# Kernel optimization log

Hardware: AMD Instinct MI355X
Metric: run time of the kernel (lower is better)

Reference implementation:

```python
import jax, jax.numpy as jnp
import numpy as np

H = 12          # heads in the ViT blocks
D = 768         # model dim (hard-coded in the module)
DFF = 3072      # mlp hidden = 4*D
ADIM = 64       # adapter bottleneck dim
L = 32          # num_latents
EPS = 1e-6      # timm ViT LayerNorm eps


def _ln(x, g, b):
    m = jnp.mean(x, axis=-1, keepdims=True)
    v = jnp.var(x, axis=-1, keepdims=True)
    return (x - m) * jax.lax.rsqrt(v + EPS) * g + b


def _quick_gelu(x):
    return x * jax.nn.sigmoid(1.702 * x)


def _sh_attn(q, k, v):
    # single-head attention used by fusion(); scale = C**-0.5 with C = full dim
    C = q.shape[-1]
    a = jax.nn.softmax(jnp.einsum('bnc,bmc->bnm', q, k) * (C ** -0.5), axis=-1)
    return jnp.einsum('bnm,bmc->bnc', a, v)


def _mhsa(x, qkv_w, qkv_b, proj_w, proj_b):
    B, N, C = x.shape
    Dh = C // H
    qkv = (x @ qkv_w.T + qkv_b).reshape(B, N, 3, H, Dh).transpose(2, 0, 3, 1, 4)
    q, k, v = qkv[0], qkv[1], qkv[2]                       # [B,H,N,Dh]
    a = jax.nn.softmax(jnp.einsum('bhnd,bhmd->bhnm', q, k) * (Dh ** -0.5), axis=-1)
    o = jnp.einsum('bhnm,bhmd->bhnd', a, v).transpose(0, 2, 1, 3).reshape(B, N, C)
    return o @ proj_w.T + proj_b


def _stream(t, ln1_g, ln1_b, qkv_w, qkv_b, proj_w, proj_b,
            ln2_g, ln2_b, fc1_w, fc1_b, fc2_w, fc2_b,
            down_w, down_b, up_w, up_b, scale):
    t = t + _mhsa(_ln(t, ln1_g, ln1_b), qkv_w, qkv_b, proj_w, proj_b)
    h = _ln(t, ln2_g, ln2_b)
    mlp = jax.nn.gelu(h @ fc1_w.T + fc1_b, approximate=False) @ fc2_w.T + fc2_b
    adapter = (_quick_gelu(h @ down_w.T + down_b) @ up_w.T + up_b) * scale
    return t + mlp + adapter


def setup_inputs() -> dict:
    key = jax.random.key(0)
    ks = iter(jax.random.split(key, 64))
    f32 = jnp.float32
    def rn(shape, std=0.02):
        return (jax.random.normal(next(ks), shape, dtype=f32) * std)
    inp = {
        'x': jax.random.normal(next(ks), (16, 512, 768), dtype=f32),
        'y': jax.random.normal(next(ks), (16, 196, 768), dtype=f32),
        'latents': rn((1, L, D)),
        'scale_a': jnp.full((1,), 0.5, f32),
        'scale_v': jnp.full((1,), 0.5, f32),
    }
    for p in ('spec', 'rgb'):
        inp.update({
            f'{p}_ln1_g': jnp.ones((D,), f32), f'{p}_ln1_b': jnp.zeros((D,), f32),
            f'{p}_qkv_w': rn((3 * D, D)), f'{p}_qkv_b': jnp.zeros((3 * D,), f32),
            f'{p}_proj_w': rn((D, D)), f'{p}_proj_b': jnp.zeros((D,), f32),
            f'{p}_ln2_g': jnp.ones((D,), f32), f'{p}_ln2_b': jnp.zeros((D,), f32),
            f'{p}_fc1_w': rn((DFF, D)), f'{p}_fc1_b': jnp.zeros((DFF,), f32),
            f'{p}_fc2_w': rn((D, DFF)), f'{p}_fc2_b': jnp.zeros((D,), f32),
            f'{p}_down_w': rn((ADIM, D)), f'{p}_down_b': jnp.zeros((ADIM,), f32),
            f'{p}_up_w': rn((D, ADIM)), f'{p}_up_b': jnp.zeros((D,), f32),
            f'{p}_scale': jnp.ones((1,), f32),
        })
    return inp


def reference(x, y, latents, scale_a, scale_v,
              spec_ln1_g, spec_ln1_b, spec_qkv_w, spec_qkv_b, spec_proj_w, spec_proj_b,
              spec_ln2_g, spec_ln2_b, spec_fc1_w, spec_fc1_b, spec_fc2_w, spec_fc2_b,
              spec_down_w, spec_down_b, spec_up_w, spec_up_b, spec_scale,
              rgb_ln1_g, rgb_ln1_b, rgb_qkv_w, rgb_qkv_b, rgb_proj_w, rgb_proj_b,
              rgb_ln2_g, rgb_ln2_b, rgb_fc1_w, rgb_fc1_b, rgb_fc2_w, rgb_fc2_b,
              rgb_down_w, rgb_down_b, rgb_up_w, rgb_up_b, rgb_scale):
    B = x.shape[0]
    # --- fusion via latent bottleneck (single-head attention) ---
    concat_ = jnp.concatenate((x, y), axis=1)                 # [B, Na+Nv, D]
    lat = jnp.broadcast_to(latents, (B, L, D))
    fused = _sh_attn(lat, concat_, concat_)                   # [B, L, D]
    x = x + scale_a * _sh_attn(x, fused, fused)
    y = y + scale_v * _sh_attn(y, fused, fused)
    # --- per-stream transformer block + adapter (dropout = eval/identity) ---
    x = _stream(x, spec_ln1_g, spec_ln1_b, spec_qkv_w, spec_qkv_b, spec_proj_w, spec_proj_b,
                spec_ln2_g, spec_ln2_b, spec_fc1_w, spec_fc1_b, spec_fc2_w, spec_fc2_b,
                spec_down_w, spec_down_b, spec_up_w, spec_up_b, spec_scale)
    y = _stream(y, rgb_ln1_g, rgb_ln1_b, rgb_qkv_w, rgb_qkv_b, rgb_proj_w, rgb_proj_b,
                rgb_ln2_g, rgb_ln2_b, rgb_fc1_w, rgb_fc1_b, rgb_fc2_w, rgb_fc2_b,
                rgb_down_w, rgb_down_b, rgb_up_w, rgb_up_b, rgb_scale)
    return (x, y)
```

## Files before the change

### kernel.cpp

```cpp
#include <hip/hip_runtime.h>
#include <hip/hip_bf16.h>


#define H_HEADS 12
#define DMODEL 768
#define DFF 3072
#define ADIM 64
#define NLAT 32
#define BATCH 16
#define NA 512
#define NV 196
#define NTOT 708
#define MCAT (BATCH * NTOT)

typedef __hip_bfloat16 bf16;
using bf16x8 = __attribute__((ext_vector_type(8))) short;
using f32x4  = __attribute__((ext_vector_type(4))) float;

static __device__ __forceinline__ float bf2f(bf16 v) { return __bfloat162float(v); }
static __device__ __forceinline__ float bflo(unsigned u) { return __uint_as_float(u << 16); }
static __device__ __forceinline__ float ld1(const float* p) { return *p; }
static __device__ __forceinline__ float ld1(const bf16* p) { return bf2f(*p); }
static __device__ __forceinline__ unsigned short f2bf_bits(float v) {
    unsigned u = __float_as_uint(v);
    return (unsigned short)((u + 0x7fffu + ((u >> 16) & 1u)) >> 16);
}

#define GLD_LDS16(gp, lp) __builtin_amdgcn_global_load_lds( \
    (const __attribute__((address_space(1))) void*)(gp), \
    (__attribute__((address_space(3))) void*)(lp), 16, 0, 0)

static inline int pad8(int v) { return (v + 7) & ~7; }

__global__ void detect_dtype_kernel(const unsigned short* __restrict__ x, int* __restrict__ flag)
{
    if (threadIdx.x == 0 && blockIdx.x == 0) {
        int big = 0;
        for (int i = 0; i < 2048; i++) {
            unsigned e = (x[i] >> 7) & 0xFF;
            if (e >= 0x90) big++;
        }
        flag[0] = (big > 16) ? 1 : 0;
        flag[1] = 0;
    }
}

template<typename TIn>
static __device__ __forceinline__ void pack_body(
    const TIn* __restrict__ x, const TIn* __restrict__ y, const TIn* __restrict__ lat,
    bf16* __restrict__ Cc, bf16* __restrict__ Lb)
{
    const int r = blockIdx.x, tid = threadIdx.x;
    const TIn* src;
    bf16* dst;
    if (r < MCAT) {
        const int b = r / NTOT, n = r - b * NTOT;
        src = (n < NA) ? x + ((size_t)(b * NA + n)) * DMODEL
                       : y + ((size_t)(b * NV + (n - NA))) * DMODEL;
        dst = Cc + (size_t)r * DMODEL;
    } else {
        src = lat + (size_t)(r - MCAT) * DMODEL;
        dst = Lb + (size_t)(r - MCAT) * DMODEL;
    }
    dst[tid]       = __float2bfloat16(ld1(src + tid));
    dst[tid + 256] = __float2bfloat16(ld1(src + tid + 256));
    dst[tid + 512] = __float2bfloat16(ld1(src + tid + 512));
}

__global__ __launch_bounds__(256)
void pack_concat_kernel(const int* __restrict__ flag, const void* x, const void* y,
                        const void* lat, bf16* __restrict__ Cc, bf16* __restrict__ Lb)
{
    if (flag[0]) pack_body<float>((const float*)x, (const float*)y, (const float*)lat, Cc, Lb);
    else         pack_body<bf16>((const bf16*)x, (const bf16*)y, (const bf16*)lat, Cc, Lb);
}

__global__ __launch_bounds__(64)
void fusion_softmax_kernel(const float* __restrict__ scores, float* __restrict__ P)
{
    const int b = blockIdx.x >> 5, l = blockIdx.x & 31, lane = threadIdx.x;
    const float* sp = scores + (size_t)b * NTOT * NLAT + l;
    float v[12];
    float mx = -1e30f;
    #pragma unroll
    for (int i = 0; i < 12; i++) {
        const int n = lane + i * 64;
        v[i] = (n < NTOT) ? sp[(size_t)n * NLAT] * 0.03608439182435161f : -1e30f;
        mx = fmaxf(mx, v[i]);
    }
    #pragma unroll
    for (int off = 32; off; off >>= 1) mx = fmaxf(mx, __shfl_xor(mx, off));
    float den = 0.f;
    #pragma unroll
    for (int i = 0; i < 12; i++) { v[i] = __expf(v[i] - mx); den += v[i]; }
    #pragma unroll
    for (int off = 32; off; off >>= 1) den += __shfl_xor(den, off);
    const float inv = 1.0f / den;
    float* op = P + ((size_t)b * NLAT + l) * 768;
    #pragma unroll
    for (int i = 0; i < 12; i++) {
        const int n = lane + i * 64;
        op[n] = (n < NTOT) ? v[i] * inv : 0.f;
    }
}

__global__ __launch_bounds__(256)
void fusion_wsum_kernel(const bf16* __restrict__ Cc, const float* __restrict__ P,
                        bf16* __restrict__ fused)
{
    const int b = blockIdx.y, d0 = blockIdx.x * 128;
    const int tid = threadIdx.x;
    const int lg = tid >> 5, dg = tid & 31;
    const int l0 = lg * 4;

    __shared__ float Ct[64][132];
    __shared__ float Ps[32][68];

    float acc[4][4] = {};

    for (int nc = 0; nc < 12; nc++) {
        const int n0 = nc * 64;
        __syncthreads();
        #pragma unroll
        for (int it = 0; it < 8; it++) {
            const int idx = it * 1024 + tid * 4;
            const int r = idx >> 7, c = idx & 127;
            const int gn = n0 + r;
            float4 v = make_float4(0.f, 0.f, 0.f, 0.f);
            if (gn < NTOT) {
                const ushort4 u = *(const ushort4*)(Cc + ((size_t)(b * NTOT + gn)) * DMODEL + d0 + c);
                v = make_float4(bflo(u.x), bflo(u.y), bflo(u.z), bflo(u.w));
            }
            Ct[r][c] = v.x; Ct[r][c + 1] = v.y; Ct[r][c + 2] = v.z; Ct[r][c + 3] = v.w;
        }
        {
            const int l = tid >> 3, off = (tid & 7) * 8;
            const float* pp = P + ((size_t)b * NLAT + l) * 768 + n0 + off;
            const float4 p0 = *(const float4*)pp;
            const float4 p1 = *(const float4*)(pp + 4);
            Ps[l][off] = p0.x; Ps[l][off + 1] = p0.y; Ps[l][off + 2] = p0.z; Ps[l][off + 3] = p0.w;
            Ps[l][off + 4] = p1.x; Ps[l][off + 5] = p1.y; Ps[l][off + 6] = p1.z; Ps[l][off + 7] = p1.w;
        }
        __syncthreads();

        for (int n = 0; n < 64; n++) {
            const float4 v = *(const float4*)&Ct[n][dg * 4];
            #pragma unroll
            for (int i = 0; i < 4; i++) {
                const float p = Ps[l0 + i][n];
                acc[i][0] += p * v.x; acc[i][1] += p * v.y;
                acc[i][2] += p * v.z; acc[i][3] += p * v.w;
            }
        }
    }

    #pragma unroll
    for (int i = 0; i < 4; i++) {
        bf16* op = fused + ((size_t)b * NLAT + l0 + i) * DMODEL + d0 + dg * 4;
        #pragma unroll
        for (int j = 0; j < 4; j++) op[j] = __float2bfloat16(acc[i][j]);
    }
}

template<typename TIn>
static __device__ __forceinline__ void attend_fused_body(
    const TIn* __restrict__ t, const bf16* __restrict__ fused,
    const TIn* __restrict__ scale_p, const TIn* __restrict__ lng, const TIn* __restrict__ lnb,
    bf16* __restrict__ out, bf16* __restrict__ hout, int Npb)
{
    const int tid = threadIdx.x;
    const int gid = blockIdx.x;
    const int b = gid / Npb;
    const TIn* row = t + (size_t)gid * DMODEL;
    const bf16* fb = fused + (size_t)b * NLAT * DMODEL;

    __shared__ float q[DMODEL];
    __shared__ float p[NLAT];
    __shared__ float rs[4], rq[4];

    for (int d = tid; d < DMODEL; d += 256) q[d] = ld1(row + d);
    __syncthreads();

    const int g = tid >> 3, li = tid & 7;
    float s = 0.f;
    const bf16* fr = fb + (size_t)g * DMODEL;
    for (int d = li; d < DMODEL; d += 8) s += q[d] * bf2f(fr[d]);
    s += __shfl_xor(s, 1); s += __shfl_xor(s, 2); s += __shfl_xor(s, 4);
    if (li == 0) p[g] = s * 0.03608439182435161f;
    __syncthreads();

    float mx = -1e30f;
    #pragma unroll
    for (int l = 0; l < NLAT; l++) mx = fmaxf(mx, p[l]);
    float w[NLAT];
    float den = 0.f;
    #pragma unroll
    for (int l = 0; l < NLAT; l++) { w[l] = __expf(p[l] - mx); den += w[l]; }
    const float sA = ld1(scale_p) / den;

    float a0 = 0.f, a1 = 0.f, a2 = 0.f;
    #pragma unroll
    for (int l = 0; l < NLAT; l++) {
        const bf16* fv = fb + (size_t)l * DMODEL;
        a0 += w[l] * bf2f(fv[tid]);
        a1 += w[l] * bf2f(fv[tid + 256]);
        a2 += w[l] * bf2f(fv[tid + 512]);
    }
    const float t0v = q[tid] + sA * a0;
    const float t1v = q[tid + 256] + sA * a1;
    const float t2v = q[tid + 512] + sA * a2;
    bf16* o = out + (size_t)gid * DMODEL;
    o[tid]       = __float2bfloat16(t0v);
    o[tid + 256] = __float2bfloat16(t1v);
    o[tid + 512] = __float2bfloat16(t2v);

    if (hout) {
        float ss = t0v + t1v + t2v;
        float sq = t0v * t0v + t1v * t1v + t2v * t2v;
        #pragma unroll
        for (int off = 32; off; off >>= 1) { ss += __shfl_xor(ss, off); sq += __shfl_xor(sq, off); }
        if ((tid & 63) == 0) { rs[tid >> 6] = ss; rq[tid >> 6] = sq; }
        __syncthreads();
        ss = rs[0] + rs[1] + rs[2] + rs[3];
        sq = rq[0] + rq[1] + rq[2] + rq[3];
        const float mean = ss * (1.0f / DMODEL);
        const float var = sq * (1.0f / DMODEL) - mean * mean;
        const float r = rsqrtf(var + 1e-6f);
        bf16* ho = hout + (size_t)gid * DMODEL;
        ho[tid]       = __float2bfloat16((t0v - mean) * r * ld1(lng + tid)       + ld1(lnb + tid));
        ho[tid + 256] = __float2bfloat16((t1v - mean) * r * ld1(lng + tid + 256) + ld1(lnb + tid + 256));
        ho[tid + 512] = __float2bfloat16((t2v - mean) * r * ld1(lng + tid + 512) + ld1(lnb + tid + 512));
    }
}

__global__ __launch_bounds__(256)
void attend_fused_kernel(const int* __restrict__ flag, const void* t, const bf16* __restrict__ fused,
                         const void* scale_p, const void* lng, const void* lnb,
                         bf16* __restrict__ out, bf16* __restrict__ hout, int Npb)
{
    if (flag[0]) attend_fused_body<float>((const float*)t, fused, (const float*)scale_p,
                                          (const float*)lng, (const float*)lnb, out, hout, Npb);
    else         attend_fused_body<bf16>((const bf16*)t, fused, (const bf16*)scale_p,
                                         (const bf16*)lng, (const bf16*)lnb, out, hout, Npb);
}

template<typename TW>
static __device__ __forceinline__ void ln_body(
    const bf16* __restrict__ in, const TW* __restrict__ g,
    const TW* __restrict__ bta, bf16* __restrict__ out)
{
    const int tid = threadIdx.x;
    const bf16* p = in + (size_t)blockIdx.x * DMODEL;
    const float v0 = bf2f(p[tid]), v1 = bf2f(p[tid + 256]), v2 = bf2f(p[tid + 512]);
    float s = v0 + v1 + v2;
    float sq = v0 * v0 + v1 * v1 + v2 * v2;
    #pragma unroll
    for (int off = 32; off; off >>= 1) { s += __shfl_xor(s, off); sq += __shfl_xor(sq, off); }
    __shared__ float rs[4], rq[4];
    if ((tid & 63) == 0) { rs[tid >> 6] = s; rq[tid >> 6] = sq; }
    __syncthreads();
    s = rs[0] + rs[1] + rs[2] + rs[3];
    sq = rq[0] + rq[1] + rq[2] + rq[3];
    const float mean = s * (1.0f / DMODEL);
    const float var = sq * (1.0f / DMODEL) - mean * mean;
    const float r = rsqrtf(var + 1e-6f);
    bf16* o = out + (size_t)blockIdx.x * DMODEL;
    o[tid]       = __float2bfloat16((v0 - mean) * r * ld1(g + tid)       + ld1(bta + tid));
    o[tid + 256] = __float2bfloat16((v1 - mean) * r * ld1(g + tid + 256) + ld1(bta + tid + 256));
    o[tid + 512] = __float2bfloat16((v2 - mean) * r * ld1(g + tid + 512) + ld1(bta + tid + 512));
}

__global__ __launch_bounds__(256)
void ln_kernel(const int* __restrict__ flag, const bf16* __restrict__ in,
               const void* g, const void* b, bf16* __restrict__ out)
{
    if (flag[0]) ln_body<float>(in, (const float*)g, (const float*)b, out);
    else         ln_body<bf16>(in, (const bf16*)g, (const bf16*)b, out);
}

__global__ __launch_bounds__(256)
void flash_attn_kernel(const bf16* __restrict__ qkv, bf16* __restrict__ o, int Npb)
{
    const int tid = threadIdx.x;
    const int wv = tid >> 6, lane = tid & 63;
    const int l15 = lane & 15, q4 = lane >> 4;
    const int h = blockIdx.x % H_HEADS, bb = blockIdx.x / H_HEADS;
    const int qt = blockIdx.y;
    const int nkv = (Npb + 63) >> 6;
    const size_t tokbase = (size_t)bb * Npb;

    __shared__ __align__(16) short Ks[64 * 64];
    __shared__ __align__(16) short Vt[64 * 64];
    __shared__ __align__(16) short Ps[4][16 * 64];

    const int qr = min(qt * 64 + wv * 16 + l15, Npb - 1);
    const bf16* qp = qkv + (tokbase + qr) * 2304 + h * 64;
    const bf16x8 qf0 = *(const bf16x8*)(const void*)(qp + q4 * 8);
    const bf16x8 qf1 = *(const bf16x8*)(const void*)(qp + 32 + q4 * 8);

    f32x4 Oa[4] = {};
    float mrow[4], lrow[4];
    #pragma unroll
    for (int i = 0; i < 4; i++) { mrow[i] = -1e30f; lrow[i] = 0.f; }

    for (int kv = 0; kv < nkv; kv++) {
        const int kv0 = kv * 64;
        __syncthreads();
        #pragma unroll
        for (int inst = 0; inst < 2; inst++) {
            const int s = inst * 256 + tid;
            const int row = s >> 3, pos = s & 7;
            const int c = pos ^ (row & 7);
            const int krc = min(kv0 + row, Npb - 1);
            GLD_LDS16(qkv + (tokbase + krc) * 2304 + DMODEL + h * 64 + c * 8, &Ks[s * 8]);
        }
        {
            const int r = tid >> 2;
            const int f0 = (tid & 3) * 16;
            const int krc = min(kv0 + r, Npb - 1);
            const short* vp = (const short*)(qkv + (tokbase + krc) * 2304 + 2 * DMODEL + h * 64 + f0);
            short vb[16];
            *(uint4*)&vb[0] = *(const uint4*)vp;
            *(uint4*)&vb[8] = *(const uint4*)(vp + 8);
            const int chunk = r >> 3, r7 = r & 7;
            #pragma unroll
            for (int j = 0; j < 16; j++) {
                const int feat = f0 + j;
                Vt[feat * 64 + (chunk ^ (feat & 7)) * 8 + r7] = vb[j];
            }
        }
        __syncthreads();

        f32x4 s4[4] = {};
        #pragma unroll
        for (int kk = 0; kk < 2; kk++) {
            const bf16x8 qf = kk ? qf1 : qf0;
            const int c = kk * 4 + q4;
            #pragma unroll
            for (int g = 0; g < 4; g++) {
                const int r = g * 16 + l15;
                const bf16x8 kf = *(const bf16x8*)(const void*)&Ks[r * 64 + (c ^ (r & 7)) * 8];
                s4[g] = __builtin_amdgcn_mfma_f32_16x16x32_bf16(qf, kf, s4[g], 0, 0, 0);
            }
        }
        float tmax[4];
        #pragma unroll
        for (int i = 0; i < 4; i++) tmax[i] = -1e30f;
        #pragma unroll
        for (int g = 0; g < 4; g++) {
            const bool valid = (kv0 + g * 16 + l15) < Npb;
            #pragma unroll
            for (int i = 0; i < 4; i++) {
                const float v = s4[g][i] * 0.125f;
                s4[g][i] = valid ? v : -1e30f;
                tmax[i] = fmaxf(tmax[i], s4[g][i]);
            }
        }
        #pragma unroll
        for (int off = 1; off < 16; off <<= 1)
            #pragma unroll
            for (int i = 0; i < 4; i++) tmax[i] = fmaxf(tmax[i], __shfl_xor(tmax[i], off));
        float alpha[4], rsum[4];
        #pragma unroll
        for (int i = 0; i < 4; i++) {
            const float mn = fmaxf(mrow[i], tmax[i]);
            alpha[i] = __expf(mrow[i] - mn);
            mrow[i] = mn;
            rsum[i] = 0.f;
        }
        #pragma unroll
        for (int g = 0; g < 4; g++) {
            const int cc = g * 16 + l15;
            const int chunk = cc >> 3;
            #pragma unroll
            for (int i = 0; i < 4; i++) {
                const int r = q4 * 4 + i;
                const float p = __expf(s4[g][i] - mrow[i]);
                rsum[i] += p;
                Ps[wv][r * 64 + (chunk ^ (r & 7)) * 8 + (cc & 7)] = (short)f2bf_bits(p);
            }
        }
        #pragma unroll
        for (int off = 1; off < 16; off <<= 1)
            #pragma unroll
            for (int i = 0; i < 4; i++) rsum[i] += __shfl_xor(rsum[i], off);
        #pragma unroll
        for (int i = 0; i < 4; i++) lrow[i] = lrow[i] * alpha[i] + rsum[i];
        #pragma unroll
        for (int g = 0; g < 4; g++)
            #pragma unroll
            for (int i = 0; i < 4; i++) Oa[g][i] *= alpha[i];

        #pragma unroll
        for (int kk = 0; kk < 2; kk++) {
            const int c = kk * 4 + q4;
            const bf16x8 pf = *(const bf16x8*)(const void*)&Ps[wv][l15 * 64 + (c ^ (l15 & 7)) * 8];
            #pragma unroll
            for (int g = 0; g < 4; g++) {
                const int feat = g * 16 + l15;
                const bf16x8 vf = *(const bf16x8*)(const void*)&Vt[feat * 64 + (c ^ (feat & 7)) * 8];
                Oa[g] = __builtin_amdgcn_mfma_f32_16x16x32_bf16(pf, vf, Oa[g], 0, 0, 0);
            }
        }
    }

    float inv[4];
    #pragma unroll
    for (int i = 0; i < 4; i++) inv[i] = 1.0f / lrow[i];
    #pragma unroll
    for (int g = 0; g < 4; g++) {
        const int colo = h * 64 + g * 16 + l15;
        #pragma unroll
        for (int i = 0; i < 4; i++) {
            const int rowg = qt * 64 + wv * 16 + q4 * 4 + i;
            if (rowg < Npb)
                o[(tokbase + rowg) * DMODEL + colo] = __float2bfloat16(Oa[g][i] * inv[i]);
        }
    }
}

template<int TM, int ACT, bool RES, bool SCALE, bool FD, typename TW>
static __device__ __forceinline__ void gemm_body(
    const bf16* __restrict__ A, const TW* __restrict__ W, const TW* __restrict__ Wd,
    const TW* __restrict__ bias, const TW* __restrict__ biasd,
    const bf16* __restrict__ resid, const TW* __restrict__ scale_p,
    void* __restrict__ C, bf16* __restrict__ Cd,
    bool cf32, int row_off, int M, int N, int K, short* As, short* Bs)
{
    const int tid = threadIdx.x;
    const int lane = tid & 63;
    const int wv = tid >> 6;
    const int l15 = lane & 15, q4 = lane >> 4;
    const int m0 = blockIdx.x * TM, n0 = blockIdx.y * 128;
    const int N1 = FD ? N - ADIM : N;
    constexpr int NF = (TM == 128) ? 4 : 2;
    const int wm = (TM == 128) ? (wv & 1) * 64 : 0;
    const int wn = (TM == 128) ? (wv >> 1) * 64 : wv * 32;

    f32x4 acc[4][NF] = {};

    for (int k0 = 0; k0 < K; k0 += 64) {
        __syncthreads();
        constexpr int AIT = TM * 8 / 256;
        #pragma unroll
        for (int it = 0; it < AIT; it++) {
            const int i = it * 256 + tid;
            const int row = i >> 3, pos = i & 7;
            const int c = pos ^ (row & 7);
            const int ra = min(m0 + row, M - 1);
            GLD_LDS16(A + (size_t)ra * K + k0 + c * 8, &As[i * 8]);
        }
        #pragma unroll
        for (int it = 0; it < 4; it++) {
            const int i = it * 256 + tid;
            const int row = i >> 3, pos = i & 7;
            const int c = pos ^ (row & 7);
            const int rb = min(n0 + row, N - 1);
            const TW* wp = (FD && rb >= N1) ? Wd + (size_t)(rb - N1) * K
                                            : W + (size_t)rb * K;
            if constexpr (sizeof(TW) == 2) {
                GLD_LDS16(wp + k0 + c * 8, &Bs[i * 8]);
            } else {
                const float* fp = (const float*)wp + k0 + c * 8;
                const float4 w0 = *(const float4*)fp;
                const float4 w1 = *(const float4*)(fp + 4);
                unsigned short hb[8];
                hb[0] = f2bf_bits(w0.x); hb[1] = f2bf_bits(w0.y);
                hb[2] = f2bf_bits(w0.z); hb[3] = f2bf_bits(w0.w);
                hb[4] = f2bf_bits(w1.x); hb[5] = f2bf_bits(w1.y);
                hb[6] = f2bf_bits(w1.z); hb[7] = f2bf_bits(w1.w);
                *(uint4*)&Bs[i * 8] = *(const uint4*)hb;
            }
        }
        __syncthreads();

        #pragma unroll
        for (int kk = 0; kk < 2; kk++) {
            bf16x8 af[4], bfr[NF];
            #pragma unroll
            for (int f = 0; f < 4; f++) {
                const int r = wm + f * 16 + l15;
                af[f] = *(const bf16x8*)(const void*)&As[(r * 8 + ((kk * 4 + q4) ^ (r & 7))) * 8];
            }
            #pragma unroll
            for (int g = 0; g < NF; g++) {
                const int rn = wn + g * 16 + l15;
                bfr[g] = *(const bf16x8*)(const void*)&Bs[(rn * 8 + ((kk * 4 + q4) ^ (rn & 7))) * 8];
            }
            #pragma unroll
            for (int f = 0; f < 4; f++)
                #pragma unroll
                for (int g = 0; g < NF; g++)
                    acc[f][g] = __builtin_amdgcn_mfma_f32_16x16x32_bf16(af[f], bfr[g], acc[f][g], 0, 0, 0);
        }
    }

    const float sc = SCALE ? ld1(scale_p) : 1.0f;
    #pragma unroll
    for (int g = 0; g < NF; g++) {
        const int colg = n0 + wn + g * 16 + l15;
        if (colg >= N) continue;
        const bool isdown = FD && (colg >= N1);
        const float bv = bias ? (isdown ? ld1(biasd + colg - N1) : ld1(bias + colg)) : 0.f;
        #pragma unroll
        for (int f = 0; f < 4; f++) {
            const int rowb = m0 + wm + f * 16 + q4 * 4;
            #pragma unroll
            for (int i = 0; i < 4; i++) {
                const int rowg = rowb + i;
                if (rowg >= M) continue;
                float v = acc[f][g][i] + bv;
                if (FD) {
                    if (isdown) v = v / (1.0f + __expf(-1.702f * v));
                    else v = 0.5f * v * (1.0f + erff(v * 0.70710678118654752f));
                } else if (ACT == 1) v = 0.5f * v * (1.0f + erff(v * 0.70710678118654752f));
                else if (ACT == 2) v = v / (1.0f + __expf(-1.702f * v));
                if (SCALE) v *= sc;
                if (RES) v += bf2f(resid[(size_t)rowg * N + colg]);
                if (FD && isdown) {
                    Cd[(size_t)rowg * ADIM + (colg - N1)] = __float2bfloat16(v);
                } else {
                    const size_t sidx = (size_t)(rowg + row_off) * N1 + colg;
                    if (cf32) ((float*)C)[sidx] = v;
                    else ((bf16*)C)[sidx] = __float2bfloat16(v);
                }
            }
        }
    }
}

template<int TM, int ACT, bool RES, bool SCALE, bool FD>
__global__ __launch_bounds__(256)
void mfma_gemm_kernel(const int* __restrict__ flag, const bf16* __restrict__ A,
                      const void* __restrict__ W, const void* __restrict__ Wd,
                      const void* __restrict__ bias, const void* __restrict__ biasd,
                      const bf16* __restrict__ resid, const void* __restrict__ sp,
                      void* __restrict__ C, bf16* __restrict__ Cd,
                      int out_mode, int row_off, int M, int N, int K)
{
    __shared__ __align__(16) short As[TM * 64];
    __shared__ __align__(16) short Bs[128 * 64];
    if (blockIdx.x * TM >= M) return;
    const bool cf32 = (out_mode == 2) || (out_mode == 1 && flag[0] != 0);
    if (flag[0])
        gemm_body<TM, ACT, RES, SCALE, FD, float>(A, (const float*)W, (const float*)Wd,
            (const float*)bias, (const float*)biasd, resid, (const float*)sp, C, Cd,
            cf32, row_off, M, N, K, As, Bs);
    else
        gemm_body<TM, ACT, RES, SCALE, FD, bf16>(A, (const bf16*)W, (const bf16*)Wd,
            (const bf16*)bias, (const bf16*)biasd, resid, (const bf16*)sp, C, Cd,
            cf32, row_off, M, N, K, As, Bs);
}

struct SW {
    const void *ln1_g, *ln1_b, *qkv_w, *qkv_b, *proj_w, *proj_b,
               *ln2_g, *ln2_b, *fc1_w, *fc1_b, *fc2_w, *fc2_b,
               *down_w, *down_b, *up_w, *up_b, *scale;
};

static void run_stream(const int* flag, bf16* t0, int M, int Npb, int nb, const SW& w,
                       bf16* h, bf16* big, bf16* ah, void* out, int out_row_off,
                       bool skip_ln1, hipStream_t s)
{
    const int mt128 = pad8((M + 127) / 128);
    const int mt64  = pad8((M + 63) / 64);
    const dim3 gqkv(mt128, 18);
    const dim3 gfc1(mt128, 25);
    const dim3 g768(mt64, 6);

    if (!skip_ln1) ln_kernel<<<M, 256, 0, s>>>(flag, t0, w.ln1_g, w.ln1_b, h);
    mfma_gemm_kernel<128, 0, false, false, false><<<gqkv, 256, 0, s>>>(
        flag, h, w.qkv_w, nullptr, w.qkv_b, nullptr, nullptr, nullptr, big, nullptr,
        0, 0, M, 2304, DMODEL);
    flash_attn_kernel<<<dim3(nb * H_HEADS, (Npb + 63) / 64), 256, 0, s>>>(big, h, Npb);
    mfma_gemm_kernel<64, 0, true, false, false><<<g768, 256, 0, s>>>(
        flag, h, w.proj_w, nullptr, w.proj_b, nullptr, t0, nullptr, t0, nullptr,
        0, 0, M, DMODEL, DMODEL);
    ln_kernel<<<M, 256, 0, s>>>(flag, t0, w.ln2_g, w.ln2_b, h);
    mfma_gemm_kernel<128, 1, false, false, true><<<gfc1, 256, 0, s>>>(
        flag, h, w.fc1_w, w.down_w, w.fc1_b, w.down_b, nullptr, nullptr, big, ah,
        0, 0, M, DFF + ADIM, DMODEL);
    mfma_gemm_kernel<64, 0, true, false, false><<<g768, 256, 0, s>>>(
        flag, big, w.fc2_w, nullptr, w.fc2_b, nullptr, t0, nullptr, t0, nullptr,
        0, 0, M, DMODEL, DFF);
    mfma_gemm_kernel<64, 0, true, true, false><<<g768, 256, 0, s>>>(
        flag, ah, w.up_w, nullptr, w.up_b, nullptr, t0, w.scale, out, nullptr,
        1, out_row_off, M, DMODEL, ADIM);
}

extern "C" void kernel_launch(void* const* d_in, const int* in_sizes, int n_in,
                              void* d_out, int out_size, void* d_ws, size_t ws_size,
                              hipStream_t stream)
{
    SW sw, rw;
    auto fill = [&](SW& s, int base) {
        s.ln1_g = d_in[base + 0];  s.ln1_b = d_in[base + 1];
        s.qkv_w = d_in[base + 2];  s.qkv_b = d_in[base + 3];
        s.proj_w = d_in[base + 4]; s.proj_b = d_in[base + 5];
        s.ln2_g = d_in[base + 6];  s.ln2_b = d_in[base + 7];
        s.fc1_w = d_in[base + 8];  s.fc1_b = d_in[base + 9];
        s.fc2_w = d_in[base + 10]; s.fc2_b = d_in[base + 11];
        s.down_w = d_in[base + 12]; s.down_b = d_in[base + 13];
        s.up_w = d_in[base + 14];  s.up_b = d_in[base + 15];
        s.scale = d_in[base + 16];
    };
    fill(sw, 5);
    fill(rw, 22);

    const int Mx = BATCH * NA;
    const int My = BATCH * NV;

    int* flag = (int*)d_ws;
    char* base = (char*)d_ws + 256;
    bf16* x1 = (bf16*)base;                base += (size_t)Mx * DMODEL * 2;
    bf16* y1 = (bf16*)base;                base += (size_t)My * DMODEL * 2;
    bf16* fused = (bf16*)base;             base += (size_t)BATCH * NLAT * DMODEL * 2;
    char* un = base;

    bf16* Cc = (bf16*)un;
    bf16* Lb = (bf16*)(un + (size_t)MCAT * DMODEL * 2);
    float* scores = (float*)(un + (size_t)(MCAT + 64) * DMODEL * 2);
    float* P = (float*)((char*)scores + (size_t)MCAT * NLAT * 4 + 256);

    const size_t stream_need_big = ((size_t)Mx * DMODEL + (size_t)Mx * DFF + (size_t)Mx * ADIM) * 2;
    const size_t fixed = 256 + ((size_t)Mx * DMODEL + (size_t)My * DMODEL + (size_t)BATCH * NLAT * DMODEL) * 2;
    const bool big_ws = ws_size >= fixed + stream_need_big;
    const int hrows = big_ws ? Mx : My;
    bf16* h  = (bf16*)un;
    bf16* big = h + (size_t)hrows * DMODEL;
    bf16* ah = big + (size_t)hrows * DFF;

    detect_dtype_kernel<<<1, 64, 0, stream>>>((const unsigned short*)d_in[0], flag);

    pack_concat_kernel<<<MCAT + NLAT, 256, 0, stream>>>(flag, d_in[0], d_in[1], d_in[2], Cc, Lb);
    mfma_gemm_kernel<128, 0, false, false, false><<<dim3(pad8((MCAT + 127) / 128), 1), 256, 0, stream>>>(
        flag + 1, Cc, Lb, nullptr, nullptr, nullptr, nullptr, nullptr, scores, nullptr,
        2, 0, MCAT, NLAT, DMODEL);
    fusion_softmax_kernel<<<BATCH * NLAT, 64, 0, stream>>>(scores, P);
    fusion_wsum_kernel<<<dim3(DMODEL / 128, BATCH), 256, 0, stream>>>(Cc, P, fused);

    attend_fused_kernel<<<BATCH * NA, 256, 0, stream>>>(
        flag, d_in[0], fused, d_in[3], sw.ln1_g, sw.ln1_b, x1, big_ws ? h : nullptr, NA);
    if (big_ws) {
        run_stream(flag, x1, Mx, NA, BATCH, sw, h, big, ah, d_out, 0, true, stream);
    } else {
        const int MCH = 2048;
        for (int c = 0; c < Mx / MCH; c++)
            run_stream(flag, x1 + (size_t)c * MCH * DMODEL, MCH, NA, MCH / NA, sw,
                       h, big, ah, d_out, c * MCH, false, stream);
    }

    attend_fused_kernel<<<BATCH * NV, 256, 0, stream>>>(
        flag, d_in[1], fused, d_in[4], rw.ln1_g, rw.ln1_b, y1, h, NV);
    run_stream(flag, y1, My, NV, BATCH, rw, h, big, ah, d_out, Mx, true, stream);
}
```

Before: 1.349 ms.

## Batch x and y streams into merged GEMM launches and stage epilogue through LDS

Concatenates the audio and visual token streams into one buffer so each GEMM, LayerNorm and MLP launch covers both. Blocks pick their weights by row index against a split point, which removes half the launches and the tail effects of the smaller y stream. The GEMM epilogue now writes through a swizzled LDS buffer, giving vectorised 4-wide coalesced stores and residual loads. The cost is a larger workspace requirement with fallback paths, plus extra LDS synchronisation in the epilogue.

```diff
diff --git a/kernel.cpp b/kernel.cpp
--- a/kernel.cpp
+++ b/kernel.cpp
@@ -12,6 +12,7 @@
 #define NV 196
 #define NTOT 708
 #define MCAT (BATCH * NTOT)
+#define MTOT (BATCH * (NA + NV))
 
 typedef __hip_bfloat16 bf16;
 using bf16x8 = __attribute__((ext_vector_type(8))) short;
@@ -272,8 +273,12 @@
 
 __global__ __launch_bounds__(256)
 void ln_kernel(const int* __restrict__ flag, const bf16* __restrict__ in,
-               const void* g, const void* b, bf16* __restrict__ out)
-{
+               const void* g0, const void* b0, const void* g1, const void* b1,
+               bf16* __restrict__ out, int split)
+{
+    const bool isY = (int)blockIdx.x >= split;
+    const void* g = isY ? g1 : g0;
+    const void* b = isY ? b1 : b0;
     if (flag[0]) ln_body<float>(in, (const float*)g, (const float*)b, out);
     else         ln_body<bf16>(in, (const bf16*)g, (const bf16*)b, out);
 }
@@ -425,7 +430,8 @@
     const TW* __restrict__ bias, const TW* __restrict__ biasd,
     const bf16* __restrict__ resid, const TW* __restrict__ scale_p,
     void* __restrict__ C, bf16* __restrict__ Cd,
-    bool cf32, int row_off, int M, int N, int K, short* As, short* Bs)
+    bool cf32, int row_off, int M, int N, int K,
+    short* As, short* Bs, float* Ep)
 {
     const int tid = threadIdx.x;
     const int lane = tid & 63;
@@ -456,8 +462,7 @@
             const int row = i >> 3, pos = i & 7;
             const int c = pos ^ (row & 7);
             const int rb = min(n0 + row, N - 1);
-            const TW* wp = (FD && rb >= N1) ? Wd + (size_t)(rb - N1) * K
-                                            : W + (size_t)rb * K;
+            const TW* wp = (FD && rb >= N1) ? Wd + (size_t)(rb - N1) * K : W + (size_t)rb * K;
             if constexpr (sizeof(TW) == 2) {
                 GLD_LDS16(wp + k0 + c * 8, &Bs[i * 8]);
             } else {
@@ -494,62 +499,101 @@
                     acc[f][g] = __builtin_amdgcn_mfma_f32_16x16x32_bf16(af[f], bfr[g], acc[f][g], 0, 0, 0);
         }
     }
+    __syncthreads();
 
     const float sc = SCALE ? ld1(scale_p) : 1.0f;
-    #pragma unroll
-    for (int g = 0; g < NF; g++) {
-        const int colg = n0 + wn + g * 16 + l15;
-        if (colg >= N) continue;
-        const bool isdown = FD && (colg >= N1);
-        const float bv = bias ? (isdown ? ld1(biasd + colg - N1) : ld1(bias + colg)) : 0.f;
-        #pragma unroll
-        for (int f = 0; f < 4; f++) {
-            const int rowb = m0 + wm + f * 16 + q4 * 4;
-            #pragma unroll
-            for (int i = 0; i < 4; i++) {
-                const int rowg = rowb + i;
-                if (rowg >= M) continue;
-                float v = acc[f][g][i] + bv;
-                if (FD) {
-                    if (isdown) v = v / (1.0f + __expf(-1.702f * v));
-                    else v = 0.5f * v * (1.0f + erff(v * 0.70710678118654752f));
-                } else if (ACT == 1) v = 0.5f * v * (1.0f + erff(v * 0.70710678118654752f));
-                else if (ACT == 2) v = v / (1.0f + __expf(-1.702f * v));
-                if (SCALE) v *= sc;
-                if (RES) v += bf2f(resid[(size_t)rowg * N + colg]);
-                if (FD && isdown) {
-                    Cd[(size_t)rowg * ADIM + (colg - N1)] = __float2bfloat16(v);
+    constexpr int NPASS = (TM == 128) ? 2 : 1;
+    #pragma unroll
+    for (int pass = 0; pass < NPASS; pass++) {
+        if (wm == pass * 64) {
+            #pragma unroll
+            for (int g = 0; g < NF; g++) {
+                const int col = wn + g * 16 + l15;
+                const int colg = n0 + col;
+                const bool isdown = FD && (colg >= N1);
+                const float bv = bias ? (isdown ? ld1(biasd + (colg - N1)) : ld1(bias + colg)) : 0.f;
+                #pragma unroll
+                for (int f = 0; f < 4; f++) {
+                    #pragma unroll
+                    for (int i = 0; i < 4; i++) {
+                        const int row = f * 16 + q4 * 4 + i;
+                        float v = acc[f][g][i] + bv;
+                        if (FD) {
+                            if (isdown) v = v / (1.0f + __expf(-1.702f * v));
+                            else v = 0.5f * v * (1.0f + erff(v * 0.70710678118654752f));
+                        } else if (ACT == 1) v = 0.5f * v * (1.0f + erff(v * 0.70710678118654752f));
+                        else if (ACT == 2) v = v / (1.0f + __expf(-1.702f * v));
+                        if (SCALE) v *= sc;
+                        const int c = col >> 2;
+                        Ep[row * 128 + (((c ^ (row & 31))) << 2) + (col & 3)] = v;
+                    }
+                }
+            }
+        }
+        __syncthreads();
+        #pragma unroll
+        for (int it = 0; it < 8; it++) {
+            const int cid = it * 256 + tid;
+            const int row = cid >> 5, c = cid & 31;
+            const int rowg = m0 + pass * 64 + row;
+            const int colg = n0 + c * 4;
+            if (rowg < M && colg < N) {
+                f32x4 v = *(const f32x4*)&Ep[row * 128 + (((c ^ (row & 31))) << 2)];
+                if (FD && colg >= N1) {
+                    ushort4 u;
+                    u.x = f2bf_bits(v[0]); u.y = f2bf_bits(v[1]);
+                    u.z = f2bf_bits(v[2]); u.w = f2bf_bits(v[3]);
+                    *(ushort4*)(Cd + (size_t)rowg * ADIM + (colg - N1)) = u;
                 } else {
-                    const size_t sidx = (size_t)(rowg + row_off) * N1 + colg;
-                    if (cf32) ((float*)C)[sidx] = v;
-                    else ((bf16*)C)[sidx] = __float2bfloat16(v);
+                    if (RES) {
+                        const ushort4 r4 = *(const ushort4*)(resid + (size_t)rowg * N + colg);
+                        v[0] += bflo(r4.x); v[1] += bflo(r4.y);
+                        v[2] += bflo(r4.z); v[3] += bflo(r4.w);
+                    }
+                    if (cf32) {
+                        *(f32x4*)((float*)C + (size_t)(rowg + row_off) * N + colg) = v;
+                    } else {
+                        ushort4 u;
+                        u.x = f2bf_bits(v[0]); u.y = f2bf_bits(v[1]);
+                        u.z = f2bf_bits(v[2]); u.w = f2bf_bits(v[3]);
+                        *(ushort4*)((bf16*)C + (size_t)(rowg + row_off) * (FD ? N1 : N) + colg) = u;
+                    }
                 }
             }
         }
+        if (pass + 1 < NPASS) __syncthreads();
     }
 }
 
 template<int TM, int ACT, bool RES, bool SCALE, bool FD>
 __global__ __launch_bounds__(256)
 void mfma_gemm_kernel(const int* __restrict__ flag, const bf16* __restrict__ A,
-                      const void* __restrict__ W, const void* __restrict__ Wd,
-                      const void* __restrict__ bias, const void* __restrict__ biasd,
-                      const bf16* __restrict__ resid, const void* __restrict__ sp,
+                      const void* W0, const void* W1, const void* Wd0, const void* Wd1,
+                      const void* b0, const void* b1, const void* bd0, const void* bd1,
+                      const bf16* __restrict__ resid, const void* sp0, const void* sp1,
                       void* __restrict__ C, bf16* __restrict__ Cd,
-                      int out_mode, int row_off, int M, int N, int K)
-{
-    __shared__ __align__(16) short As[TM * 64];
-    __shared__ __align__(16) short Bs[128 * 64];
-    if (blockIdx.x * TM >= M) return;
+                      int out_mode, int row_off, int M, int N, int K, int split)
+{
+    __shared__ __align__(16) char SMEM[32768];
+    if ((int)blockIdx.x * TM >= M) return;
+    const bool isY = ((int)blockIdx.x * TM) >= split;
+    const void* W = isY ? W1 : W0;
+    const void* Wd = isY ? Wd1 : Wd0;
+    const void* bb = isY ? b1 : b0;
+    const void* bd = isY ? bd1 : bd0;
+    const void* sp = isY ? sp1 : sp0;
+    short* As = (short*)SMEM;
+    short* Bs = As + TM * 64;
+    float* Ep = (float*)SMEM;
     const bool cf32 = (out_mode == 2) || (out_mode == 1 && flag[0] != 0);
     if (flag[0])
         gemm_body<TM, ACT, RES, SCALE, FD, float>(A, (const float*)W, (const float*)Wd,
-            (const float*)bias, (const float*)biasd, resid, (const float*)sp, C, Cd,
-            cf32, row_off, M, N, K, As, Bs);
+            (const float*)bb, (const float*)bd, resid, (const float*)sp, C, Cd,
+            cf32, row_off, M, N, K, As, Bs, Ep);
     else
         gemm_body<TM, ACT, RES, SCALE, FD, bf16>(A, (const bf16*)W, (const bf16*)Wd,
-            (const bf16*)bias, (const bf16*)biasd, resid, (const bf16*)sp, C, Cd,
-            cf32, row_off, M, N, K, As, Bs);
+            (const bf16*)bb, (const bf16*)bd, resid, (const bf16*)sp, C, Cd,
+            cf32, row_off, M, N, K, As, Bs, Ep);
 }
 
 struct SW {
@@ -558,34 +602,35 @@
                *down_w, *down_b, *up_w, *up_b, *scale;
 };
 
-static void run_stream(const int* flag, bf16* t0, int M, int Npb, int nb, const SW& w,
-                       bf16* h, bf16* big, bf16* ah, void* out, int out_row_off,
-                       bool skip_ln1, hipStream_t s)
-{
-    const int mt128 = pad8((M + 127) / 128);
-    const int mt64  = pad8((M + 63) / 64);
-    const dim3 gqkv(mt128, 18);
-    const dim3 gfc1(mt128, 25);
-    const dim3 g768(mt64, 6);
-
-    if (!skip_ln1) ln_kernel<<<M, 256, 0, s>>>(flag, t0, w.ln1_g, w.ln1_b, h);
-    mfma_gemm_kernel<128, 0, false, false, false><<<gqkv, 256, 0, s>>>(
-        flag, h, w.qkv_w, nullptr, w.qkv_b, nullptr, nullptr, nullptr, big, nullptr,
-        0, 0, M, 2304, DMODEL);
-    flash_attn_kernel<<<dim3(nb * H_HEADS, (Npb + 63) / 64), 256, 0, s>>>(big, h, Npb);
-    mfma_gemm_kernel<64, 0, true, false, false><<<g768, 256, 0, s>>>(
-        flag, h, w.proj_w, nullptr, w.proj_b, nullptr, t0, nullptr, t0, nullptr,
-        0, 0, M, DMODEL, DMODEL);
-    ln_kernel<<<M, 256, 0, s>>>(flag, t0, w.ln2_g, w.ln2_b, h);
-    mfma_gemm_kernel<128, 1, false, false, true><<<gfc1, 256, 0, s>>>(
-        flag, h, w.fc1_w, w.down_w, w.fc1_b, w.down_b, nullptr, nullptr, big, ah,
-        0, 0, M, DFF + ADIM, DMODEL);
-    mfma_gemm_kernel<64, 0, true, false, false><<<g768, 256, 0, s>>>(
-        flag, big, w.fc2_w, nullptr, w.fc2_b, nullptr, t0, nullptr, t0, nullptr,
-        0, 0, M, DMODEL, DFF);
-    mfma_gemm_kernel<64, 0, true, true, false><<<g768, 256, 0, s>>>(
-        flag, ah, w.up_w, nullptr, w.up_b, nullptr, t0, w.scale, out, nullptr,
-        1, out_row_off, M, DMODEL, ADIM);
+static void stream_seq(const int* flag, bf16* t0, bf16* h, bf16* big, bf16* ah,
+                       int M, int split, const SW& a, const SW& b,
+                       void* outC, int row_off,
+                       int npb0, int rows0, int npb1, int rows1, hipStream_t s)
+{
+    const dim3 gq(pad8((M + 127) / 128), 18);
+    const dim3 gf(pad8((M + 127) / 128), 25);
+    const dim3 g7(pad8((M + 63) / 64), 6);
+
+    mfma_gemm_kernel<128, 0, false, false, false><<<gq, 256, 0, s>>>(flag, h,
+        a.qkv_w, b.qkv_w, nullptr, nullptr, a.qkv_b, b.qkv_b, nullptr, nullptr,
+        nullptr, nullptr, nullptr, big, nullptr, 0, 0, M, 2304, DMODEL, split);
+    flash_attn_kernel<<<dim3((rows0 / npb0) * H_HEADS, (npb0 + 63) / 64), 256, 0, s>>>(big, h, npb0);
+    if (rows1)
+        flash_attn_kernel<<<dim3((rows1 / npb1) * H_HEADS, (npb1 + 63) / 64), 256, 0, s>>>(
+            big + (size_t)rows0 * 2304, h + (size_t)rows0 * DMODEL, npb1);
+    mfma_gemm_kernel<64, 0, true, false, false><<<g7, 256, 0, s>>>(flag, h,
+        a.proj_w, b.proj_w, nullptr, nullptr, a.proj_b, b.proj_b, nullptr, nullptr,
+        t0, nullptr, nullptr, t0, nullptr, 0, 0, M, DMODEL, DMODEL, split);
+    ln_kernel<<<M, 256, 0, s>>>(flag, t0, a.ln2_g, a.ln2_b, b.ln2_g, b.ln2_b, h, split);
+    mfma_gemm_kernel<128, 1, false, false, true><<<gf, 256, 0, s>>>(flag, h,
+        a.fc1_w, b.fc1_w, a.down_w, b.down_w, a.fc1_b, b.fc1_b, a.down_b, b.down_b,
+        nullptr, nullptr, nullptr, big, ah, 0, 0, M, DFF + ADIM, DMODEL, split);
+    mfma_gemm_kernel<64, 0, true, false, false><<<g7, 256, 0, s>>>(flag, big,
+        a.fc2_w, b.fc2_w, nullptr, nullptr, a.fc2_b, b.fc2_b, nullptr, nullptr,
+        t0, nullptr, nullptr, t0, nullptr, 0, 0, M, DMODEL, DFF, split);
+    mfma_gemm_kernel<64, 0, true, true, false><<<g7, 256, 0, s>>>(flag, ah,
+        a.up_w, b.up_w, nullptr, nullptr, a.up_b, b.up_b, nullptr, nullptr,
+        t0, a.scale, b.scale, outC, nullptr, 1, row_off, M, DMODEL, ADIM, split);
 }
 
 extern "C" void kernel_launch(void* const* d_in, const int* in_sizes, int n_in,
@@ -609,48 +654,105 @@
 
     const int Mx = BATCH * NA;
     const int My = BATCH * NV;
+    const int NOSPLIT = 1 << 30;
+
+    const size_t szA = 256 + ((size_t)MTOT * DMODEL * 2 + (size_t)BATCH * NLAT * DMODEL
+                     + (size_t)MTOT * DFF + (size_t)MTOT * ADIM) * 2;
+    const size_t szB = 256 + ((size_t)Mx * DMODEL * 2 + (size_t)My * DMODEL
+                     + (size_t)BATCH * NLAT * DMODEL + (size_t)Mx * DFF + (size_t)Mx * ADIM) * 2;
 
     int* flag = (int*)d_ws;
-    char* base = (char*)d_ws + 256;
-    bf16* x1 = (bf16*)base;                base += (size_t)Mx * DMODEL * 2;
-    bf16* y1 = (bf16*)base;                base += (size_t)My * DMODEL * 2;
-    bf16* fused = (bf16*)base;             base += (size_t)BATCH * NLAT * DMODEL * 2;
-    char* un = base;
-
-    bf16* Cc = (bf16*)un;
-    bf16* Lb = (bf16*)(un + (size_t)MCAT * DMODEL * 2);
-    float* scores = (float*)(un + (size_t)(MCAT + 64) * DMODEL * 2);
-    float* P = (float*)((char*)scores + (size_t)MCAT * NLAT * 4 + 256);
-
-    const size_t stream_need_big = ((size_t)Mx * DMODEL + (size_t)Mx * DFF + (size_t)Mx * ADIM) * 2;
-    const size_t fixed = 256 + ((size_t)Mx * DMODEL + (size_t)My * DMODEL + (size_t)BATCH * NLAT * DMODEL) * 2;
-    const bool big_ws = ws_size >= fixed + stream_need_big;
-    const int hrows = big_ws ? Mx : My;
-    bf16* h  = (bf16*)un;
-    bf16* big = h + (size_t)hrows * DMODEL;
-    bf16* ah = big + (size_t)hrows * DFF;
-
     detect_dtype_kernel<<<1, 64, 0, stream>>>((const unsigned short*)d_in[0], flag);
 
-    pack_concat_kernel<<<MCAT + NLAT, 256, 0, stream>>>(flag, d_in[0], d_in[1], d_in[2], Cc, Lb);
-    mfma_gemm_kernel<128, 0, false, false, false><<<dim3(pad8((MCAT + 127) / 128), 1), 256, 0, stream>>>(
-        flag + 1, Cc, Lb, nullptr, nullptr, nullptr, nullptr, nullptr, scores, nullptr,
-        2, 0, MCAT, NLAT, DMODEL);
-    fusion_softmax_kernel<<<BATCH * NLAT, 64, 0, stream>>>(scores, P);
-    fusion_wsum_kernel<<<dim3(DMODEL / 128, BATCH), 256, 0, stream>>>(Cc, P, fused);
-
-    attend_fused_kernel<<<BATCH * NA, 256, 0, stream>>>(
-        flag, d_in[0], fused, d_in[3], sw.ln1_g, sw.ln1_b, x1, big_ws ? h : nullptr, NA);
-    if (big_ws) {
-        run_stream(flag, x1, Mx, NA, BATCH, sw, h, big, ah, d_out, 0, true, stream);
+    if (ws_size >= szA) {
+        char* base = (char*)d_ws + 256;
+        bf16* t0 = (bf16*)base;      base += (size_t)MTOT * DMODEL * 2;
+        bf16* fused = (bf16*)base;   base += (size_t)BATCH * NLAT * DMODEL * 2;
+        bf16* h = (bf16*)base;       base += (size_t)MTOT * DMODEL * 2;
+        bf16* big = (bf16*)base;     base += (size_t)MTOT * DFF * 2;
+        bf16* ah = (bf16*)base;
+
+        bf16* Cc = h;
+        bf16* Lb = ah;
+        float* scores = (float*)big;
+        float* P = (float*)((char*)big + 2 * 1024 * 1024);
+
+        pack_concat_kernel<<<MCAT + NLAT, 256, 0, stream>>>(flag, d_in[0], d_in[1], d_in[2], Cc, Lb);
+        mfma_gemm_kernel<128, 0, false, false, false><<<dim3(pad8((MCAT + 127) / 128), 1), 256, 0, stream>>>(
+            flag + 1, Cc, Lb, Lb, nullptr, nullptr, nullptr, nullptr, nullptr, nullptr,
+            nullptr, nullptr, nullptr, scores, nullptr, 2, 0, MCAT, NLAT, DMODEL, NOSPLIT);
+        fusion_softmax_kernel<<<BATCH * NLAT, 64, 0, stream>>>(scores, P);
+        fusion_wsum_kernel<<<dim3(DMODEL / 128, BATCH), 256, 0, stream>>>(Cc, P, fused);
+
+        attend_fused_kernel<<<BATCH * NA, 256, 0, stream>>>(
+            flag, d_in[0], fused, d_in[3], sw.ln1_g, sw.ln1_b, t0, h, NA);
+        attend_fused_kernel<<<BATCH * NV, 256, 0, stream>>>(
+            flag, d_in[1], fused, d_in[4], rw.ln1_g, rw.ln1_b,
+            t0 + (size_t)Mx * DMODEL, h + (size_t)Mx * DMODEL, NV);
+
+        stream_seq(flag, t0, h, big, ah, MTOT, Mx, sw, rw, d_out, 0,
+                   NA, Mx, NV, My, stream);
+    } else if (ws_size >= szB) {
+        char* base = (char*)d_ws + 256;
+        bf16* x1 = (bf16*)base;      base += (size_t)Mx * DMODEL * 2;
+        bf16* y1 = (bf16*)base;      base += (size_t)My * DMODEL * 2;
+        bf16* fused = (bf16*)base;   base += (size_t)BATCH * NLAT * DMODEL * 2;
+        bf16* h = (bf16*)base;       base += (size_t)Mx * DMODEL * 2;
+        bf16* big = (bf16*)base;     base += (size_t)Mx * DFF * 2;
+        bf16* ah = (bf16*)base;
+
+        bf16* Cc = big;
+        bf16* Lb = ah;
+        float* scores = (float*)((char*)big + 18 * 1024 * 1024);
+        float* P = (float*)((char*)big + 20 * 1024 * 1024);
+
+        pack_concat_kernel<<<MCAT + NLAT, 256, 0, stream>>>(flag, d_in[0], d_in[1], d_in[2], Cc, Lb);
+        mfma_gemm_kernel<128, 0, false, false, false><<<dim3(pad8((MCAT + 127) / 128), 1), 256, 0, stream>>>(
+            flag + 1, Cc, Lb, Lb, nullptr, nullptr, nullptr, nullptr, nullptr, nullptr,
+            nullptr, nullptr, nullptr, scores, nullptr, 2, 0, MCAT, NLAT, DMODEL, NOSPLIT);
+        fusion_softmax_kernel<<<BATCH * NLAT, 64, 0, stream>>>(scores, P);
+        fusion_wsum_kernel<<<dim3(DMODEL / 128, BATCH), 256, 0, stream>>>(Cc, P, fused);
+
+        attend_fused_kernel<<<BATCH * NA, 256, 0, stream>>>(
+            flag, d_in[0], fused, d_in[3], sw.ln1_g, sw.ln1_b, x1, h, NA);
+        stream_seq(flag, x1, h, big, ah, Mx, NOSPLIT, sw, sw, d_out, 0, NA, Mx, 0, 0, stream);
+
+        attend_fused_kernel<<<BATCH * NV, 256, 0, stream>>>(
+            flag, d_in[1], fused, d_in[4], rw.ln1_g, rw.ln1_b, y1, h, NV);
+        stream_seq(flag, y1, h, big, ah, My, NOSPLIT, rw, rw, d_out, Mx, NV, My, 0, 0, stream);
     } else {
+        char* base = (char*)d_ws + 256;
+        bf16* x1 = (bf16*)base;      base += (size_t)Mx * DMODEL * 2;
+        bf16* y1 = (bf16*)base;      base += (size_t)My * DMODEL * 2;
+        bf16* fused = (bf16*)base;   base += (size_t)BATCH * NLAT * DMODEL * 2;
+        bf16* h = (bf16*)base;       base += (size_t)My * DMODEL * 2;
+        bf16* big = (bf16*)base;     base += (size_t)My * DFF * 2;
+        bf16* ah = (bf16*)base;
+
+        bf16* Cc = big;
+        bf16* Lb = ah;
+        float* scores = (float*)((char*)big + 17500160);
+        float* P = (float*)h;
+
+        pack_concat_kernel<<<MCAT + NLAT, 256, 0, stream>>>(flag, d_in[0], d_in[1], d_in[2], Cc, Lb);
+        mfma_gemm_kernel<128, 0, false, false, false><<<dim3(pad8((MCAT + 127) / 128), 1), 256, 0, stream>>>(
+            flag + 1, Cc, Lb, Lb, nullptr, nullptr, nullptr, nullptr, nullptr, nullptr,
+            nullptr, nullptr, nullptr, scores, nullptr, 2, 0, MCAT, NLAT, DMODEL, NOSPLIT);
+        fusion_softmax_kernel<<<BATCH * NLAT, 64, 0, stream>>>(scores, P);
+        fusion_wsum_kernel<<<dim3(DMODEL / 128, BATCH), 256, 0, stream>>>(Cc, P, fused);
+
+        attend_fused_kernel<<<BATCH * NA, 256, 0, stream>>>(
+            flag, d_in[0], fused, d_in[3], sw.ln1_g, sw.ln1_b, x1, nullptr, NA);
         const int MCH = 2048;
-        for (int c = 0; c < Mx / MCH; c++)
-            run_stream(flag, x1 + (size_t)c * MCH * DMODEL, MCH, NA, MCH / NA, sw,
-                       h, big, ah, d_out, c * MCH, false, stream);
-    }
-
-    attend_fused_kernel<<<BATCH * NV, 256, 0, stream>>>(
-        flag, d_in[1], fused, d_in[4], rw.ln1_g, rw.ln1_b, y1, h, NV);
-    run_stream(flag, y1, My, NV, BATCH, rw, h, big, ah, d_out, Mx, true, stream);
-}
+        for (int c = 0; c < Mx / MCH; c++) {
+            bf16* t0c = x1 + (size_t)c * MCH * DMODEL;
+            ln_kernel<<<MCH, 256, 0, stream>>>(flag, t0c, sw.ln1_g, sw.ln1_b,
+                                               sw.ln1_g, sw.ln1_b, h, NOSPLIT);
+            stream_seq(flag, t0c, h, big, ah, MCH, NOSPLIT, sw, sw, d_out, c * MCH,
+                       NA, MCH, 0, 0, stream);
+        }
+        attend_fused_kernel<<<BATCH * NV, 256, 0, stream>>>(
+            flag, d_in[1], fused, d_in[4], rw.ln1_g, rw.ln1_b, y1, h, NV);
+        stream_seq(flag, y1, h, big, ah, My, NOSPLIT, rw, rw, d_out, Mx, NV, My, 0, 0, stream);
+    }
+}
```

Measured after the change: 1.205 ms. 10.6% less time.
